# Kernel optimization log

Measured on AMD Instinct MI355X. Metric: run time of the kernel, lower is better.

## Reference

```python
import jax, jax.numpy as jnp
import numpy as np

DIM = 4096
N_HEADS = 32
HEAD_DIM = 128
N_KV = 8
REP = N_HEADS // N_KV  # 4
B = 8       # number of packed sequences (block-diagonal blocks)
S = 1024    # tokens per sequence
T = B * S   # seqlen_sum = 8192


def setup_inputs() -> dict:
    key = jax.random.key(0)
    ks = jax.random.split(key, 6)
    x = jax.random.normal(ks[0], (T, DIM), dtype=jnp.float32)
    # RoPE freqs: positions restart at 0 for each packed sequence
    pos = jnp.tile(jnp.arange(S, dtype=jnp.float32), B)            # [T]
    inv_freq = 1.0 / (10000.0 ** (jnp.arange(0, HEAD_DIM, 2, dtype=jnp.float32) / HEAD_DIM))  # [HEAD_DIM//2]
    freqs = pos[:, None] * inv_freq[None, :]                       # [T, HEAD_DIM//2]
    cos = jnp.cos(freqs)
    sin = jnp.sin(freqs)
    s = 0.02
    wq = jax.random.normal(ks[1], (DIM, N_HEADS * HEAD_DIM), dtype=jnp.float32) * s
    wk = jax.random.normal(ks[2], (DIM, N_KV * HEAD_DIM), dtype=jnp.float32) * s
    wv = jax.random.normal(ks[3], (DIM, N_KV * HEAD_DIM), dtype=jnp.float32) * s
    wo = jax.random.normal(ks[4], (N_HEADS * HEAD_DIM, DIM), dtype=jnp.float32) * s
    return {"x": x, "cos": cos, "sin": sin, "wq": wq, "wk": wk, "wv": wv, "wo": wo}


def _rope(t, cos, sin):
    # t: [T, H, D]; cos/sin: [T, D//2]; complex rotation on (even, odd) pairs
    th, hd = t.shape[1], t.shape[2]
    tp = t.reshape(t.shape[0], th, hd // 2, 2)
    te, to = tp[..., 0], tp[..., 1]
    c = cos[:, None, :]
    s = sin[:, None, :]
    oe = te * c - to * s
    oo = te * s + to * c
    return jnp.stack([oe, oo], axis=-1).reshape(t.shape)


def reference(x, cos, sin, wq, wk, wv, wo):
    scale = HEAD_DIM ** -0.5
    q = (x @ wq).reshape(T, N_HEADS, HEAD_DIM)
    k = (x @ wk).reshape(T, N_KV, HEAD_DIM)
    v = (x @ wv).reshape(T, N_KV, HEAD_DIM)
    q = _rope(q, cos, sin)
    k = _rope(k, cos, sin)
    # Block-diagonal mask with equal blocks == batched attention over B sequences.
    # GQA: q head index h = kv*REP + r (matches repeat_interleave on kv dim),
    # so group q heads as [N_KV, REP] instead of materializing repeated K/V.
    q = q.reshape(B, S, N_KV, REP, HEAD_DIM)
    k = k.reshape(B, S, N_KV, HEAD_DIM)
    v = v.reshape(B, S, N_KV, HEAD_DIM)
    scores = jnp.einsum('bqkrd,bskd->bkrqs', q, k) * scale   # [B, N_KV, REP, S, S]
    attn = jax.nn.softmax(scores, axis=-1)
    out = jnp.einsum('bkrqs,bskd->bqkrd', attn, v)           # [B, S, N_KV, REP, D]
    out = out.reshape(T, N_HEADS * HEAD_DIM)
    return out @ wo
```

## Files before the change

kernel.cpp:

```cpp
#include <hip/hip_runtime.h>
#include <math.h>

typedef unsigned short ushort_t;
typedef __attribute__((ext_vector_type(8))) short short8;
typedef __attribute__((ext_vector_type(4))) float f32x4;

#define MFMA16(a, b, c) __builtin_amdgcn_mfma_f32_16x16x32_bf16(a, b, c, 0, 0, 0)

__device__ __forceinline__ ushort_t f2bf(float f) {
    union { float f; unsigned u; } v;
    v.f = f;
    unsigned r = v.u + 0x7FFF + ((v.u >> 16) & 1);
    return (ushort_t)(r >> 16);
}

__device__ __forceinline__ void gload_lds16(const ushort_t* g, ushort_t* l) {
    __builtin_amdgcn_global_load_lds(
        (const __attribute__((address_space(1))) void*)g,
        (__attribute__((address_space(3))) void*)l, 16, 0, 0);
}

__global__ __launch_bounds__(256) void cast_f32_bf16(const float* __restrict__ src,
                                                     ushort_t* __restrict__ dst, int n8) {
    int i = blockIdx.x * 256 + threadIdx.x;
    if (i >= n8) return;
    const float4* s = (const float4*)src;
    float4 a = s[2 * i], b = s[2 * i + 1];
    union { ushort_t u[8]; uint4 v; } o;
    o.u[0] = f2bf(a.x); o.u[1] = f2bf(a.y); o.u[2] = f2bf(a.z); o.u[3] = f2bf(a.w);
    o.u[4] = f2bf(b.x); o.u[5] = f2bf(b.y); o.u[6] = f2bf(b.z); o.u[7] = f2bf(b.w);
    ((uint4*)dst)[i] = o.v;
}

__global__ __launch_bounds__(256) void transpose_cast(const float* __restrict__ src,
                                                      int D, int N,
                                                      ushort_t* __restrict__ dst, int dstStride) {
    __shared__ float t[32][33];
    int n0 = blockIdx.x * 32, d0 = blockIdx.y * 32;
    int tx = threadIdx.x & 31, ty = threadIdx.x >> 5;
#pragma unroll
    for (int i = 0; i < 4; i++)
        t[ty + 8 * i][tx] = src[(size_t)(d0 + ty + 8 * i) * N + n0 + tx];
    __syncthreads();
#pragma unroll
    for (int i = 0; i < 4; i++) {
        int n = ty + 8 * i;
        dst[(size_t)(n0 + n) * dstStride + d0 + tx] = f2bf(t[tx][n]);
    }
}

__global__ __launch_bounds__(256) void transpose_v(const ushort_t* __restrict__ qkv,
                                                   ushort_t* __restrict__ vt) {
    __shared__ ushort_t t[32][33];
    int bk = blockIdx.z; int b = bk >> 3, kvh = bk & 7;
    int s0 = blockIdx.x * 32, d0 = blockIdx.y * 32;
    int tx = threadIdx.x & 31, ty = threadIdx.x >> 5;
#pragma unroll
    for (int i = 0; i < 4; i++)
        t[ty + 8 * i][tx] = qkv[(size_t)(b * 1024 + s0 + ty + 8 * i) * 6144 + 5120 + kvh * 128 + d0 + tx];
    __syncthreads();
#pragma unroll
    for (int i = 0; i < 4; i++)
        vt[((size_t)(b * 8 + kvh) * 128 + d0 + ty + 8 * i) * 1024 + s0 + tx] = t[tx][ty + 8 * i];
}

template <int EPI>
__global__ __launch_bounds__(512, 2) void gemm9(
    const ushort_t* __restrict__ A, const ushort_t* __restrict__ Bt,
    ushort_t* __restrict__ obf, float* __restrict__ of32,
    int M, int N, int K,
    const float* __restrict__ cosT, const float* __restrict__ sinT) {
    extern __shared__ __align__(16) ushort_t lds[];
    const int tid = threadIdx.x;
    const int lane = tid & 63, wv = tid >> 6;
    const int wr = wv >> 2, wc = wv & 3;
    const int lr = lane & 15, g = lane >> 4;

    const int gx = gridDim.x;
    const int nwg = gx * gridDim.y;
    const int bid = blockIdx.y * gx + blockIdx.x;
    const int swz = (bid & 7) * (nwg >> 3) + (bid >> 3);
    const int brow = (swz / gx) * 256, bcol = (swz % gx) * 256;

    const int st_r = tid >> 3, st_p = tid & 7;
    const int cA = (st_p ^ (st_r & 7)) * 8;
    const size_t aS0 = (size_t)(brow + st_r) * K + cA;
    const size_t bS0 = (size_t)(bcol + st_r) * K + cA;
    const int dstT = st_r * 64 + st_p * 8;

    const int sl0 = (g ^ (lr & 7)) * 8;
    const int sl1 = ((4 + g) ^ (lr & 7)) * 8;
    const int aRow = (wr * 128 + lr) * 64;
    const int bRow = (wc * 64 + lr) * 64;

    f32x4 acc[8][4];
#pragma unroll
    for (int m = 0; m < 8; m++)
#pragma unroll
        for (int n = 0; n < 4; n++) acc[m][n] = (f32x4){0.f, 0.f, 0.f, 0.f};

#define STG_A(kn, roff)                                                          \
    gload_lds16(A + aS0 + (size_t)(roff) * K + (size_t)(kn) * 64,                \
                lds + ((kn) % 3) * 16384 + (roff) * 64 + dstT)
#define STG_B(kn, roff)                                                          \
    gload_lds16(Bt + bS0 + (size_t)(roff) * K + (size_t)(kn) * 64,               \
                lds + 49152 + ((kn) & 1) * 16384 + (roff) * 64 + dstT)

    STG_A(0, 0); STG_A(0, 64); STG_A(0, 128); STG_A(0, 192);
    STG_B(0, 0); STG_B(0, 64); STG_B(0, 128); STG_B(0, 192);
    STG_A(1, 0); STG_A(1, 64); STG_A(1, 128); STG_A(1, 192);
    asm volatile("s_waitcnt vmcnt(4)" ::: "memory");
    __builtin_amdgcn_s_barrier();

    const int NKT = K >> 6;
    for (int kt = 0; kt < NKT; ++kt) {
        const int sa = (kt % 3) * 16384;
        const int sb = 49152 + (kt & 1) * 16384;
        const bool stgB = kt < NKT - 1;
        const bool stgA = kt < NKT - 2;
        short8 bfr[4], af[4];

#pragma unroll
        for (int n = 0; n < 4; ++n)
            bfr[n] = *(const short8*)(lds + sb + bRow + n * 1024 + sl0);
#pragma unroll
        for (int m = 0; m < 4; ++m)
            af[m] = *(const short8*)(lds + sa + aRow + m * 1024 + sl0);
        if (stgB) { STG_B(kt + 1, 0); STG_B(kt + 1, 64); }
        __builtin_amdgcn_s_barrier();
        asm volatile("s_waitcnt lgkmcnt(0)" ::: "memory");
        __builtin_amdgcn_sched_barrier(0);
        __builtin_amdgcn_s_setprio(1);
#pragma unroll
        for (int m = 0; m < 4; ++m)
#pragma unroll
            for (int n = 0; n < 4; ++n)
                acc[m][n] = MFMA16(af[m], bfr[n], acc[m][n]);
        __builtin_amdgcn_s_setprio(0);
        __builtin_amdgcn_s_barrier();

#pragma unroll
        for (int m = 0; m < 4; ++m)
            af[m] = *(const short8*)(lds + sa + aRow + 4096 + m * 1024 + sl0);
        if (stgB) { STG_B(kt + 1, 128); STG_B(kt + 1, 192); }
        __builtin_amdgcn_s_barrier();
        asm volatile("s_waitcnt lgkmcnt(0)" ::: "memory");
        __builtin_amdgcn_sched_barrier(0);
        __builtin_amdgcn_s_setprio(1);
#pragma unroll
        for (int m = 0; m < 4; ++m)
#pragma unroll
            for (int n = 0; n < 4; ++n)
                acc[m + 4][n] = MFMA16(af[m], bfr[n], acc[m + 4][n]);
        __builtin_amdgcn_s_setprio(0);
        __builtin_amdgcn_s_barrier();

#pragma unroll
        for (int n = 0; n < 4; ++n)
            bfr[n] = *(const short8*)(lds + sb + bRow + n * 1024 + sl1);
#pragma unroll
        for (int m = 0; m < 4; ++m)
            af[m] = *(const short8*)(lds + sa + aRow + m * 1024 + sl1);
        if (stgA) { STG_A(kt + 2, 0); STG_A(kt + 2, 64); }
        __builtin_amdgcn_s_barrier();
        asm volatile("s_waitcnt lgkmcnt(0)" ::: "memory");
        __builtin_amdgcn_sched_barrier(0);
        __builtin_amdgcn_s_setprio(1);
#pragma unroll
        for (int m = 0; m < 4; ++m)
#pragma unroll
            for (int n = 0; n < 4; ++n)
                acc[m][n] = MFMA16(af[m], bfr[n], acc[m][n]);
        __builtin_amdgcn_s_setprio(0);
        __builtin_amdgcn_s_barrier();

#pragma unroll
        for (int m = 0; m < 4; ++m)
            af[m] = *(const short8*)(lds + sa + aRow + 4096 + m * 1024 + sl1);
        if (stgA) { STG_A(kt + 2, 128); STG_A(kt + 2, 192); }
        if (kt < NKT - 2)       asm volatile("s_waitcnt vmcnt(4)" ::: "memory");
        else if (kt == NKT - 2) asm volatile("s_waitcnt vmcnt(0)" ::: "memory");
        __builtin_amdgcn_s_barrier();
        asm volatile("s_waitcnt lgkmcnt(0)" ::: "memory");
        __builtin_amdgcn_sched_barrier(0);
        __builtin_amdgcn_s_setprio(1);
#pragma unroll
        for (int m = 0; m < 4; ++m)
#pragma unroll
            for (int n = 0; n < 4; ++n)
                acc[m + 4][n] = MFMA16(af[m], bfr[n], acc[m + 4][n]);
        __builtin_amdgcn_s_setprio(0);
        __builtin_amdgcn_s_barrier();
    }
#undef STG_A
#undef STG_B

#pragma unroll
    for (int m = 0; m < 8; ++m) {
#pragma unroll
        for (int n = 0; n < 4; ++n) {
#pragma unroll
            for (int reg = 0; reg < 4; ++reg) {
                int r = brow + wr * 128 + m * 16 + g * 4 + reg;
                int c = bcol + wc * 64 + n * 16 + lr;
                float val = acc[m][n][reg];
                if (EPI == 1) {
                    float other = __shfl_xor(val, 1, 64);
                    if (c < 5120) {
                        int pos = r & 1023;
                        int pair = (c & 127) >> 1;
                        float cz = cosT[pos * 64 + pair];
                        float sz = sinT[pos * 64 + pair];
                        val = val * cz + other * ((c & 1) ? sz : -sz);
                        if (c < 4096) val *= 0.12752551286084110f;
                    }
                    obf[(size_t)r * N + c] = f2bf(val);
                } else {
                    of32[(size_t)r * N + c] = val;
                }
            }
        }
    }
}

__global__ __launch_bounds__(512, 2) void attn_fwd2(const ushort_t* __restrict__ qkv,
                                                    const ushort_t* __restrict__ vt,
                                                    ushort_t* __restrict__ aout) {
    extern __shared__ __align__(16) ushort_t lds[];
    const int tid = threadIdx.x, lane = tid & 63, w = tid >> 6;
    const int lr = lane & 15, g = lane >> 4;
    const int hr = w & 3, qc = w >> 2;
    const int qt = blockIdx.x, kvh = blockIdx.y, b = blockIdx.z;
    const int h = kvh * 4 + hr;
    const size_t qRow0 = (size_t)b * 1024 + qt * 64 + qc * 32;
    const size_t kBase = (size_t)b * 1024 * 6144 + 4096 + kvh * 128;
    const size_t vBase = (size_t)(b * 8 + kvh) * 128 * 1024;
    ushort_t* Pw = lds + 32768 + w * 2304;

    short8 qf[2][4];
#pragma unroll
    for (int qg = 0; qg < 2; ++qg)
#pragma unroll
        for (int kd = 0; kd < 4; ++kd)
            qf[qg][kd] = *(const short8*)&qkv[(qRow0 + qg * 16 + lr) * 6144 + h * 128 + kd * 32 + g * 8];

    f32x4 o[2][8];
#pragma unroll
    for (int qg = 0; qg < 2; ++qg)
#pragma unroll
        for (int nd = 0; nd < 8; ++nd) o[qg][nd] = (f32x4){0.f, 0.f, 0.f, 0.f};
    f32x4 lsum[2];
    lsum[0] = (f32x4){0.f, 0.f, 0.f, 0.f};
    lsum[1] = (f32x4){0.f, 0.f, 0.f, 0.f};

#define STAGE_KV(kt)                                                                   \
    {                                                                                  \
        const int buf_ = (kt) & 1;                                                     \
        {                                                                              \
            const int r0_ = tid >> 4, p_ = tid & 15;                                   \
            gload_lds16(qkv + kBase + (size_t)((kt) * 64 + r0_) * 6144 + ((p_ ^ (r0_ & 7)) * 8), \
                        lds + buf_ * 8192 + r0_ * 128 + p_ * 8);                       \
            const int r1_ = r0_ + 32;                                                  \
            gload_lds16(qkv + kBase + (size_t)((kt) * 64 + r1_) * 6144 + ((p_ ^ (r1_ & 7)) * 8), \
                        lds + buf_ * 8192 + r1_ * 128 + p_ * 8);                       \
        }                                                                              \
        {                                                                              \
            const int d0_ = tid >> 3, p_ = tid & 7;                                    \
            gload_lds16(vt + vBase + (size_t)d0_ * 1024 + (kt) * 64 + ((p_ ^ (d0_ & 7)) * 8), \
                        lds + 16384 + buf_ * 8192 + d0_ * 64 + p_ * 8);                \
            const int d1_ = d0_ + 64;                                                  \
            gload_lds16(vt + vBase + (size_t)d1_ * 1024 + (kt) * 64 + ((p_ ^ (d1_ & 7)) * 8), \
                        lds + 16384 + buf_ * 8192 + d1_ * 64 + p_ * 8);                \
        }                                                                              \
    }

    STAGE_KV(0);

    for (int kt = 0; kt < 16; ++kt) {
        const int buf = kt & 1;
        if (kt < 15) {
            STAGE_KV(kt + 1);
            asm volatile("s_waitcnt vmcnt(4)" ::: "memory");
        } else {
            asm volatile("s_waitcnt vmcnt(0)" ::: "memory");
        }
        __builtin_amdgcn_s_barrier();

        f32x4 sc[2][4];
#pragma unroll
        for (int qg = 0; qg < 2; ++qg)
#pragma unroll
            for (int ns = 0; ns < 4; ++ns) sc[qg][ns] = (f32x4){0.f, 0.f, 0.f, 0.f};
        __builtin_amdgcn_s_setprio(1);
#pragma unroll
        for (int ns = 0; ns < 4; ++ns) {
            const int key = ns * 16 + lr;
#pragma unroll
            for (int kd = 0; kd < 4; ++kd) {
                const short8 kf = *(const short8*)(lds + buf * 8192 + key * 128 +
                                                   (((kd * 4 + g) ^ (lr & 7)) * 8));
                sc[0][ns] = MFMA16(qf[0][kd], kf, sc[0][ns]);
                sc[1][ns] = MFMA16(qf[1][kd], kf, sc[1][ns]);
            }
        }
        __builtin_amdgcn_s_setprio(0);

#pragma unroll
        for (int qg = 0; qg < 2; ++qg) {
#pragma unroll
            for (int ns = 0; ns < 4; ++ns) {
#pragma unroll
                for (int j = 0; j < 4; ++j) {
                    float p = exp2f(sc[qg][ns][j]);
                    sc[qg][ns][j] = p;
                    lsum[qg][j] += p;
                }
            }
        }
#pragma unroll
        for (int qg = 0; qg < 2; ++qg)
#pragma unroll
            for (int ns = 0; ns < 4; ++ns)
#pragma unroll
                for (int j = 0; j < 4; ++j)
                    Pw[(qg * 16 + g * 4 + j) * 72 + ns * 16 + lr] = f2bf(sc[qg][ns][j]);

        __builtin_amdgcn_s_setprio(1);
#pragma unroll
        for (int ks = 0; ks < 2; ++ks) {
            short8 pa[2];
            pa[0] = *(const short8*)(Pw + (0 + lr) * 72 + ks * 32 + g * 8);
            pa[1] = *(const short8*)(Pw + (16 + lr) * 72 + ks * 32 + g * 8);
#pragma unroll
            for (int nd = 0; nd < 8; ++nd) {
                const int d = nd * 16 + lr;
                const short8 vf = *(const short8*)(lds + 16384 + buf * 8192 + d * 64 +
                                                   (((ks * 4 + g) ^ (d & 7)) * 8));
                o[0][nd] = MFMA16(pa[0], vf, o[0][nd]);
                o[1][nd] = MFMA16(pa[1], vf, o[1][nd]);
            }
        }
        __builtin_amdgcn_s_setprio(0);
        __builtin_amdgcn_s_barrier();
    }
#undef STAGE_KV

#pragma unroll
    for (int qg = 0; qg < 2; ++qg) {
#pragma unroll
        for (int j = 0; j < 4; ++j) {
            float s = lsum[qg][j];
            s += __shfl_xor(s, 1, 64);
            s += __shfl_xor(s, 2, 64);
            s += __shfl_xor(s, 4, 64);
            s += __shfl_xor(s, 8, 64);
            const float inv = 1.0f / s;
            const size_t r = qRow0 + qg * 16 + g * 4 + j;
#pragma unroll
            for (int nd = 0; nd < 8; ++nd)
                aout[r * 4096 + h * 128 + nd * 16 + lr] = f2bf(o[qg][nd][j] * inv);
        }
    }
}

extern "C" void kernel_launch(void* const* d_in, const int* in_sizes, int n_in,
                              void* d_out, int out_size, void* d_ws, size_t ws_size,
                              hipStream_t stream) {
    const float* x    = (const float*)d_in[0];
    const float* cosT = (const float*)d_in[1];
    const float* sinT = (const float*)d_in[2];
    const float* wq   = (const float*)d_in[3];
    const float* wk   = (const float*)d_in[4];
    const float* wv   = (const float*)d_in[5];
    const float* wo   = (const float*)d_in[6];
    float* out = (float*)d_out;

    char* ws = (char*)d_ws;
    ushort_t* xb   = (ushort_t*)(ws);
    ushort_t* wT   = (ushort_t*)(ws + 67108864);
    ushort_t* woT  = (ushort_t*)(ws + 117440512);
    ushort_t* qkv  = (ushort_t*)(ws + 150994944);
    ushort_t* vtb  = (ushort_t*)(ws + 67108864);
    ushort_t* attn = (ushort_t*)(ws);

    hipFuncSetAttribute((const void*)gemm9<1>, hipFuncAttributeMaxDynamicSharedMemorySize, 163840);
    hipFuncSetAttribute((const void*)gemm9<2>, hipFuncAttributeMaxDynamicSharedMemorySize, 163840);
    hipFuncSetAttribute((const void*)attn_fwd2, hipFuncAttributeMaxDynamicSharedMemorySize, 102400);

    cast_f32_bf16<<<16384, 256, 0, stream>>>(x, xb, 8192 * 4096 / 8);
    transpose_cast<<<dim3(128, 128), 256, 0, stream>>>(wq, 4096, 4096, wT, 4096);
    transpose_cast<<<dim3(32, 128), 256, 0, stream>>>(wk, 4096, 1024, wT + (size_t)4096 * 4096, 4096);
    transpose_cast<<<dim3(32, 128), 256, 0, stream>>>(wv, 4096, 1024, wT + (size_t)5120 * 4096, 4096);
    transpose_cast<<<dim3(128, 128), 256, 0, stream>>>(wo, 4096, 4096, woT, 4096);

    gemm9<1><<<dim3(24, 32), 512, 163840, stream>>>(xb, wT, qkv, nullptr, 8192, 6144, 4096, cosT, sinT);
    transpose_v<<<dim3(32, 4, 64), 256, 0, stream>>>(qkv, vtb);
    attn_fwd2<<<dim3(16, 8, 8), 512, 102400, stream>>>(qkv, vtb, attn);
    gemm9<2><<<dim3(16, 32), 512, 163840, stream>>>(attn, woT, nullptr, out, 8192, 4096, 4096, nullptr, nullptr);
}
```

Baseline: 950.3 us.

## Collapse GEMM main loop to one barrier per k-tile with upfront prefetch

Restructures the GEMM k-loop so each iteration waits on global loads and barriers once, issues all prefetches for the next B tile and the A tile two steps ahead at the top, then runs all four MFMA phases without intermediate barriers or priority toggles. This removes the eight barriers, four lgkmcnt waits and setprio switches per k-tile in the older ping-pong schedule. In exchange it keeps an extra set of B fragments live and leaves LDS-read/MFMA interleaving to the compiler, which may raise register pressure or lose the explicit overlap between waves.

```diff
diff --git a/kernel.cpp b/kernel.cpp
--- a/kernel.cpp
+++ b/kernel.cpp
@@ -65,7 +65,7 @@
 }
 
 template <int EPI>
-__global__ __launch_bounds__(512, 2) void gemm9(
+__global__ __launch_bounds__(512, 2) void gemm10(
     const ushort_t* __restrict__ A, const ushort_t* __restrict__ Bt,
     ushort_t* __restrict__ obf, float* __restrict__ of32,
     int M, int N, int K,
@@ -99,98 +99,83 @@
 #pragma unroll
         for (int n = 0; n < 4; n++) acc[m][n] = (f32x4){0.f, 0.f, 0.f, 0.f};
 
-#define STG_A(kn, roff)                                                          \
-    gload_lds16(A + aS0 + (size_t)(roff) * K + (size_t)(kn) * 64,                \
-                lds + ((kn) % 3) * 16384 + (roff) * 64 + dstT)
-#define STG_B(kn, roff)                                                          \
-    gload_lds16(Bt + bS0 + (size_t)(roff) * K + (size_t)(kn) * 64,               \
-                lds + 49152 + ((kn) & 1) * 16384 + (roff) * 64 + dstT)
-
-    STG_A(0, 0); STG_A(0, 64); STG_A(0, 128); STG_A(0, 192);
-    STG_B(0, 0); STG_B(0, 64); STG_B(0, 128); STG_B(0, 192);
-    STG_A(1, 0); STG_A(1, 64); STG_A(1, 128); STG_A(1, 192);
-    asm volatile("s_waitcnt vmcnt(4)" ::: "memory");
-    __builtin_amdgcn_s_barrier();
+#define STG_A(kn)                                                                \
+    {                                                                            \
+        const int s_ = ((kn) % 3) * 16384;                                       \
+        gload_lds16(A + aS0 + (size_t)(kn) * 64, lds + s_ + dstT);               \
+        gload_lds16(A + aS0 + (size_t)64 * K + (size_t)(kn) * 64,                \
+                    lds + s_ + 4096 + dstT);                                     \
+        gload_lds16(A + aS0 + (size_t)128 * K + (size_t)(kn) * 64,               \
+                    lds + s_ + 8192 + dstT);                                     \
+        gload_lds16(A + aS0 + (size_t)192 * K + (size_t)(kn) * 64,               \
+                    lds + s_ + 12288 + dstT);                                    \
+    }
+#define STG_B(kn)                                                                \
+    {                                                                            \
+        const int s_ = 49152 + ((kn) & 1) * 16384;                               \
+        gload_lds16(Bt + bS0 + (size_t)(kn) * 64, lds + s_ + dstT);              \
+        gload_lds16(Bt + bS0 + (size_t)64 * K + (size_t)(kn) * 64,               \
+                    lds + s_ + 4096 + dstT);                                     \
+        gload_lds16(Bt + bS0 + (size_t)128 * K + (size_t)(kn) * 64,              \
+                    lds + s_ + 8192 + dstT);                                     \
+        gload_lds16(Bt + bS0 + (size_t)192 * K + (size_t)(kn) * 64,              \
+                    lds + s_ + 12288 + dstT);                                    \
+    }
+
+    STG_A(0); STG_B(0); STG_A(1);
 
     const int NKT = K >> 6;
     for (int kt = 0; kt < NKT; ++kt) {
         const int sa = (kt % 3) * 16384;
         const int sb = 49152 + (kt & 1) * 16384;
-        const bool stgB = kt < NKT - 1;
-        const bool stgA = kt < NKT - 2;
-        short8 bfr[4], af[4];
-
+
+        if (kt == NKT - 1) asm volatile("s_waitcnt vmcnt(0)" ::: "memory");
+        else               asm volatile("s_waitcnt vmcnt(4)" ::: "memory");
+        __builtin_amdgcn_s_barrier();
+        __builtin_amdgcn_sched_barrier(0);
+
+        if (kt < NKT - 1) STG_B(kt + 1);
+        if (kt < NKT - 2) STG_A(kt + 2);
+
+        short8 bfr0[4], bfr1[4], af[4];
 #pragma unroll
         for (int n = 0; n < 4; ++n)
-            bfr[n] = *(const short8*)(lds + sb + bRow + n * 1024 + sl0);
+            bfr0[n] = *(const short8*)(lds + sb + bRow + n * 1024 + sl0);
 #pragma unroll
         for (int m = 0; m < 4; ++m)
             af[m] = *(const short8*)(lds + sa + aRow + m * 1024 + sl0);
-        if (stgB) { STG_B(kt + 1, 0); STG_B(kt + 1, 64); }
-        __builtin_amdgcn_s_barrier();
-        asm volatile("s_waitcnt lgkmcnt(0)" ::: "memory");
-        __builtin_amdgcn_sched_barrier(0);
-        __builtin_amdgcn_s_setprio(1);
 #pragma unroll
         for (int m = 0; m < 4; ++m)
 #pragma unroll
             for (int n = 0; n < 4; ++n)
-                acc[m][n] = MFMA16(af[m], bfr[n], acc[m][n]);
-        __builtin_amdgcn_s_setprio(0);
-        __builtin_amdgcn_s_barrier();
-
+                acc[m][n] = MFMA16(af[m], bfr0[n], acc[m][n]);
 #pragma unroll
         for (int m = 0; m < 4; ++m)
             af[m] = *(const short8*)(lds + sa + aRow + 4096 + m * 1024 + sl0);
-        if (stgB) { STG_B(kt + 1, 128); STG_B(kt + 1, 192); }
-        __builtin_amdgcn_s_barrier();
-        asm volatile("s_waitcnt lgkmcnt(0)" ::: "memory");
-        __builtin_amdgcn_sched_barrier(0);
-        __builtin_amdgcn_s_setprio(1);
 #pragma unroll
         for (int m = 0; m < 4; ++m)
 #pragma unroll
             for (int n = 0; n < 4; ++n)
-                acc[m + 4][n] = MFMA16(af[m], bfr[n], acc[m + 4][n]);
-        __builtin_amdgcn_s_setprio(0);
-        __builtin_amdgcn_s_barrier();
-
+                acc[m + 4][n] = MFMA16(af[m], bfr0[n], acc[m + 4][n]);
 #pragma unroll
         for (int n = 0; n < 4; ++n)
-            bfr[n] = *(const short8*)(lds + sb + bRow + n * 1024 + sl1);
+            bfr1[n] = *(const short8*)(lds + sb + bRow + n * 1024 + sl1);
 #pragma unroll
         for (int m = 0; m < 4; ++m)
             af[m] = *(const short8*)(lds + sa + aRow + m * 1024 + sl1);
-        if (stgA) { STG_A(kt + 2, 0); STG_A(kt + 2, 64); }
-        __builtin_amdgcn_s_barrier();
-        asm volatile("s_waitcnt lgkmcnt(0)" ::: "memory");
-        __builtin_amdgcn_sched_barrier(0);
-        __builtin_amdgcn_s_setprio(1);
 #pragma unroll
         for (int m = 0; m < 4; ++m)
 #pragma unroll
             for (int n = 0; n < 4; ++n)
-                acc[m][n] = MFMA16(af[m], bfr[n], acc[m][n]);
-        __builtin_amdgcn_s_setprio(0);
-        __builtin_amdgcn_s_barrier();
-
+                acc[m][n] = MFMA16(af[m], bfr1[n], acc[m][n]);
 #pragma unroll
         for (int m = 0; m < 4; ++m)
             af[m] = *(const short8*)(lds + sa + aRow + 4096 + m * 1024 + sl1);
-        if (stgA) { STG_A(kt + 2, 128); STG_A(kt + 2, 192); }
-        if (kt < NKT - 2)       asm volatile("s_waitcnt vmcnt(4)" ::: "memory");
-        else if (kt == NKT - 2) asm volatile("s_waitcnt vmcnt(0)" ::: "memory");
-        __builtin_amdgcn_s_barrier();
-        asm volatile("s_waitcnt lgkmcnt(0)" ::: "memory");
-        __builtin_amdgcn_sched_barrier(0);
-        __builtin_amdgcn_s_setprio(1);
 #pragma unroll
         for (int m = 0; m < 4; ++m)
 #pragma unroll
             for (int n = 0; n < 4; ++n)
-                acc[m + 4][n] = MFMA16(af[m], bfr[n], acc[m + 4][n]);
-        __builtin_amdgcn_s_setprio(0);
-        __builtin_amdgcn_s_barrier();
+                acc[m + 4][n] = MFMA16(af[m], bfr1[n], acc[m + 4][n]);
     }
 #undef STG_A
 #undef STG_B
@@ -383,8 +368,8 @@
     ushort_t* vtb  = (ushort_t*)(ws + 67108864);
     ushort_t* attn = (ushort_t*)(ws);
 
-    hipFuncSetAttribute((const void*)gemm9<1>, hipFuncAttributeMaxDynamicSharedMemorySize, 163840);
-    hipFuncSetAttribute((const void*)gemm9<2>, hipFuncAttributeMaxDynamicSharedMemorySize, 163840);
+    hipFuncSetAttribute((const void*)gemm10<1>, hipFuncAttributeMaxDynamicSharedMemorySize, 163840);
+    hipFuncSetAttribute((const void*)gemm10<2>, hipFuncAttributeMaxDynamicSharedMemorySize, 163840);
     hipFuncSetAttribute((const void*)attn_fwd2, hipFuncAttributeMaxDynamicSharedMemorySize, 102400);
 
     cast_f32_bf16<<<16384, 256, 0, stream>>>(x, xb, 8192 * 4096 / 8);
@@ -393,8 +378,8 @@
     transpose_cast<<<dim3(32, 128), 256, 0, stream>>>(wv, 4096, 1024, wT + (size_t)5120 * 4096, 4096);
     transpose_cast<<<dim3(128, 128), 256, 0, stream>>>(wo, 4096, 4096, woT, 4096);
 
-    gemm9<1><<<dim3(24, 32), 512, 163840, stream>>>(xb, wT, qkv, nullptr, 8192, 6144, 4096, cosT, sinT);
+    gemm10<1><<<dim3(24, 32), 512, 163840, stream>>>(xb, wT, qkv, nullptr, 8192, 6144, 4096, cosT, sinT);
     transpose_v<<<dim3(32, 4, 64), 256, 0, stream>>>(qkv, vtb);
     attn_fwd2<<<dim3(16, 8, 8), 512, 102400, stream>>>(qkv, vtb, attn);
-    gemm9<2><<<dim3(16, 32), 512, 163840, stream>>>(attn, woT, nullptr, out, 8192, 4096, 4096, nullptr, nullptr);
-}
+    gemm10<2><<<dim3(16, 32), 512, 163840, stream>>>(attn, woT, nullptr, out, 8192, 4096, 4096, nullptr, nullptr);
+}
```

After: 951.5 us. No clear change (+0.1%).
